# Kernel optimization log

Hardware: AMD Instinct MI355X
Metric: run time of the kernel (lower is better)

## Reference

```python
import jax, jax.numpy as jnp
import numpy as np

N_NODES = 50000
N_EDGES = 600000
D_IN = 128
D_OUT = 128


def setup_inputs() -> dict:
    key = jax.random.key(0)
    k1, k2, k3, k4 = jax.random.split(key, 4)
    x = jax.random.normal(k1, (N_NODES, D_IN), dtype=jnp.float32)
    edge_index = jax.random.randint(k2, (2, N_EDGES), 0, N_NODES, dtype=jnp.int64)
    edge_weight = jax.random.uniform(k3, (N_EDGES,), dtype=jnp.float32)
    W = jax.random.normal(k4, (D_IN, D_OUT), dtype=jnp.float32) * (1.0 / np.sqrt(D_IN))
    b = jnp.zeros((D_OUT,), dtype=jnp.float32)
    return {"x": x, "edge_index": edge_index, "edge_weight": edge_weight, "W": W, "b": b}


def reference(x, edge_index, edge_weight, W, b):
    # GCNConv (PyG semantics): add self-loops, symmetric deg^{-1/2} normalization,
    # linear transform, scatter-add to targets, bias; then ReLU. Dropout is
    # identity in eval mode.
    n = x.shape[0]
    loop = jnp.arange(n, dtype=edge_index.dtype)
    src = jnp.concatenate([edge_index[0], loop])  # message sources
    dst = jnp.concatenate([edge_index[1], loop])  # aggregation targets
    ew = jnp.concatenate([edge_weight, jnp.ones((n,), dtype=x.dtype)])
    # weighted in-degree on targets
    deg = jax.ops.segment_sum(ew, dst, num_segments=n)
    dinv = jnp.where(deg > 0, jax.lax.rsqrt(deg), jnp.zeros_like(deg))
    norm = dinv[src] * ew * dinv[dst]  # [E+N]
    h = x @ W  # [N, D_OUT]
    msg = h[src] * norm[:, None]  # [E+N, D_OUT]
    out = jax.ops.segment_sum(msg, dst, num_segments=n) + b
    return jax.nn.relu(out)
```

## Files before the change

### kernel.cpp

```cpp
#include <hip/hip_runtime.h>

#define N_NODES 50000
#define N_EDGES 600000
#define D 128
#define SCAN_B 256
#define NB ((N_NODES + SCAN_B - 1) / SCAN_B)
#define REP 4
#define FXSHIFT 44
#define GEMM_BLOCKS ((N_NODES + 63) / 64)
#define FILL_BLOCKS ((N_EDGES + 255) / 256)
#define ZERO_BLOCKS 392

typedef __attribute__((ext_vector_type(8))) short short8;
typedef __attribute__((ext_vector_type(4))) float f32x4;
typedef unsigned long long u64;

__device__ __forceinline__ ushort f2bf(float f) {
    unsigned u = __float_as_uint(f);
    unsigned r = (u + 0x7FFFu + ((u >> 16) & 1u)) >> 16;
    return (ushort)r;
}
__device__ __forceinline__ float bf2f(ushort h) {
    return __uint_as_float(((unsigned)h) << 16);
}

__device__ __forceinline__ void wfrag_body(int t, const float* __restrict__ W,
                                           ushort* __restrict__ wfh,
                                           ushort* __restrict__ wfl) {
    int lane = t & 63;
    int ks   = (t >> 6) & 3;
    int ct   = t >> 8;
    int n  = ct * 16 + (lane & 15);
    int k0 = ks * 32 + (lane >> 4) * 8;
    ushort hv[8], lv[8];
#pragma unroll
    for (int j = 0; j < 8; ++j) {
        float v = W[(k0 + j) * D + n];
        ushort hh = f2bf(v);
        hv[j] = hh;
        lv[j] = f2bf(v - bf2f(hh));
    }
    size_t base = (((size_t)ct * 4 + ks) * 64 + lane) * 8;
#pragma unroll
    for (int j = 0; j < 8; ++j) { wfh[base + j] = hv[j]; wfl[base + j] = lv[j]; }
}

__global__ void prep_kernel(ulonglong2* __restrict__ zp, int n2,
                            const float* __restrict__ W,
                            ushort* __restrict__ wfh, ushort* __restrict__ wfl) {
    if (blockIdx.x < ZERO_BLOCKS) {
        int i = blockIdx.x * 256 + threadIdx.x;
        if (i < n2) zp[i] = make_ulonglong2(0ull, 0ull);
    } else {
        wfrag_body((blockIdx.x - ZERO_BLOCKS) * 256 + threadIdx.x, W, wfh, wfl);
    }
}

__global__ void deg_cnt_kernel(const int* __restrict__ dst,
                               const float* __restrict__ ew,
                               u64* __restrict__ degp) {
    int e = blockIdx.x * 256 + threadIdx.x;
    if (e < N_EDGES) {
        int d = dst[e];
        int r = blockIdx.x & (REP - 1);
        u64 fx = (u64)llrintf(ew[e] * 16777216.0f);
        atomicAdd(&degp[(size_t)d * REP + r], (1ull << FXSHIFT) | fx);
    }
}

__global__ void scan_fused_kernel(const u64* __restrict__ degp,
                                  float* __restrict__ dinv,
                                  int* __restrict__ off,
                                  int* __restrict__ cursor,
                                  u64* __restrict__ flags) {
    __shared__ int s[SCAN_B];
    __shared__ int sbase_sh;
    int t = threadIdx.x;
    int i = blockIdx.x * SCAN_B + t;
    int v = 0;
    u64 pr[REP];
    if (i < N_NODES) {
        u64 fxsum = 0;
        int c = 0;
        const u64* dp = degp + (size_t)i * REP;
#pragma unroll
        for (int r = 0; r < REP; ++r) {
            pr[r] = dp[r];
            fxsum += pr[r] & ((1ull << FXSHIFT) - 1);
            c += (int)(pr[r] >> FXSHIFT);
        }
        float deg = 1.0f + (float)fxsum * (1.0f / 16777216.0f);
        dinv[i] = rsqrtf(deg);
        v = c;
    }
    s[t] = v;
    __syncthreads();
    for (int o = 1; o < SCAN_B; o <<= 1) {
        int x = (t >= o) ? s[t - o] : 0;
        __syncthreads();
        s[t] += x;
        __syncthreads();
    }
    int localExcl = s[t] - v;
    int blockSum  = s[SCAN_B - 1];

    if (t == 0) {
        __hip_atomic_store(&flags[blockIdx.x], (1ull << 62) | (u64)blockSum,
                           __ATOMIC_RELEASE, __HIP_MEMORY_SCOPE_AGENT);
    }
    if (t < 64) {
        u64 sum = 0;
        for (int j0 = 0; j0 < (int)blockIdx.x; j0 += 64) {
            int j = j0 + t;
            u64 f = 0;
            if (j < (int)blockIdx.x) {
                do {
                    f = __hip_atomic_load(&flags[j], __ATOMIC_ACQUIRE,
                                          __HIP_MEMORY_SCOPE_AGENT);
                } while (f == 0ull);
            }
            sum += f & ((1ull << 62) - 1);
        }
#pragma unroll
        for (int o = 32; o > 0; o >>= 1)
            sum += (u64)__shfl_xor((long long)sum, o);
        if (t == 0) sbase_sh = (int)sum;
    }
    __syncthreads();

    if (i < N_NODES) {
        int o = localExcl + sbase_sh;
        off[i] = o;
        int run = o;
        int* cp = cursor + (size_t)i * REP;
#pragma unroll
        for (int r = 0; r < REP; ++r) {
            cp[r] = run;
            run += (int)(pr[r] >> FXSHIFT);
        }
    }
    if (i == 0) off[N_NODES] = N_EDGES;
}

__global__ __launch_bounds__(256) void fused_fg_kernel(
        const float* __restrict__ x,
        const ushort* __restrict__ wfh, const ushort* __restrict__ wfl,
        ushort* __restrict__ hbf,
        const int* __restrict__ src, const int* __restrict__ dst,
        const float* __restrict__ ew, const float* __restrict__ dinv,
        int* __restrict__ cursor, u64* __restrict__ edge_s) {
    __shared__ __attribute__((aligned(16))) ushort xh[64 * 128];

    int t = threadIdx.x;
    int b = blockIdx.x;
    if (b < GEMM_BLOCKS) {
        int r0 = b * 64;
#pragma unroll
        for (int p = 0; p < 8; ++p) {
            int row  = p * 8 + (t >> 5);
            int g    = t & 31;
            int grow = r0 + row;
            float4 v = make_float4(0.f, 0.f, 0.f, 0.f);
            if (grow < N_NODES) v = ((const float4*)(x + (size_t)grow * D))[g];
            ushort4 hi;
            hi.x = f2bf(v.x); hi.y = f2bf(v.y); hi.z = f2bf(v.z); hi.w = f2bf(v.w);
            int bo = (row * 256 + g * 8) ^ ((row & 7) << 4);
            *(ushort4*)((char*)xh + bo) = hi;
        }
        __syncthreads();

        int w  = t >> 6;
        int l  = t & 63;
        int m  = l & 15;
        int gq = l >> 4;

        f32x4 acc[8];
#pragma unroll
        for (int ct = 0; ct < 8; ++ct) acc[ct] = (f32x4){0.f, 0.f, 0.f, 0.f};

#pragma unroll
        for (int ks = 0; ks < 4; ++ks) {
            int row = w * 16 + m;
            int bo  = (row * 256 + gq * 16 + ks * 64) ^ ((row & 7) << 4);
            short8 ah = *(const short8*)((const char*)xh + bo);
#pragma unroll
            for (int ct = 0; ct < 8; ++ct) {
                size_t fb = (((size_t)ct * 4 + ks) * 64 + l) * 8;
                short8 bh = *(const short8*)(wfh + fb);
                short8 bl = *(const short8*)(wfl + fb);
                acc[ct] = __builtin_amdgcn_mfma_f32_16x16x32_bf16(ah, bh, acc[ct], 0, 0, 0);
                acc[ct] = __builtin_amdgcn_mfma_f32_16x16x32_bf16(ah, bl, acc[ct], 0, 0, 0);
            }
        }

        int orow0 = r0 + w * 16 + gq * 4;
#pragma unroll
        for (int ct = 0; ct < 8; ++ct) {
#pragma unroll
            for (int r = 0; r < 4; ++r) {
                int row = orow0 + r;
                if (row < N_NODES) hbf[(size_t)row * D + ct * 16 + m] = f2bf(acc[ct][r]);
            }
        }
    } else {
        int fb = b - GEMM_BLOCKS;
        int e = fb * 256 + t;
        if (e >= N_EDGES) return;
        int s = src[e];
        int d = dst[e];
        int r = fb & (REP - 1);
        int pos = atomicAdd(&cursor[(size_t)d * REP + r], 1);
        float w = ew[e] * dinv[s] * dinv[d];
        edge_s[pos] = ((u64)__float_as_uint(w) << 32) | (unsigned)s;
    }
}

__global__ __launch_bounds__(256) void gather_kernel(
        const int* __restrict__ off, const u64* __restrict__ edge_s,
        const float* __restrict__ dinv,
        const ushort* __restrict__ hbf, const float* __restrict__ b,
        float* __restrict__ out) {
    int node = blockIdx.x * 4 + (threadIdx.x >> 6);
    if (node >= N_NODES) return;
    int lane = threadIdx.x & 63;
    int q  = lane >> 4;
    int fl = lane & 15;

    int begin = off[node];
    int end   = off[node + 1];
    float dd  = dinv[node];
    float sw  = dd * dd;

    float acc[8] = {0.f, 0.f, 0.f, 0.f, 0.f, 0.f, 0.f, 0.f};

    short8 sv = ((const short8*)(hbf + (size_t)node * D))[fl];
    if (q == 0) {
#pragma unroll
        for (int j = 0; j < 8; ++j) acc[j] = bf2f((ushort)sv[j]) * sw;
    }

    for (int j0 = begin; j0 < end; j0 += 64) {
        int nc = end - j0;
        if (nc > 64) nc = 64;
        u64 p = 0;
        if (lane < nc) p = edge_s[j0 + lane];
        int iters = (nc + 3) >> 2;
#pragma unroll 2
        for (int t = 0; t < iters; ++t) {
            int ei = t * 4 + q;
            u64 pe = __shfl((long long)p, ei);
            bool valid = ei < nc;
            int   ss = valid ? (int)(pe & 0xFFFFFFFFu) : 0;
            float ww = valid ? __uint_as_float((unsigned)(pe >> 32)) : 0.0f;
            short8 v = ((const short8*)(hbf + (size_t)ss * D))[fl];
#pragma unroll
            for (int j = 0; j < 8; ++j)
                acc[j] = fmaf(bf2f((ushort)v[j]), ww, acc[j]);
        }
    }

#pragma unroll
    for (int j = 0; j < 8; ++j) {
        acc[j] += __shfl_xor(acc[j], 16);
        acc[j] += __shfl_xor(acc[j], 32);
    }

    if (q == 0) {
        float4 b1 = ((const float4*)b)[fl * 2];
        float4 b2 = ((const float4*)b)[fl * 2 + 1];
        float4 o1 = make_float4(fmaxf(acc[0] + b1.x, 0.f), fmaxf(acc[1] + b1.y, 0.f),
                                fmaxf(acc[2] + b1.z, 0.f), fmaxf(acc[3] + b1.w, 0.f));
        float4 o2 = make_float4(fmaxf(acc[4] + b2.x, 0.f), fmaxf(acc[5] + b2.y, 0.f),
                                fmaxf(acc[6] + b2.z, 0.f), fmaxf(acc[7] + b2.w, 0.f));
        ((float4*)(out + (size_t)node * D))[fl * 2]     = o1;
        ((float4*)(out + (size_t)node * D))[fl * 2 + 1] = o2;
    }
}

__global__ void fb_init_kernel(float* __restrict__ deg) {
    int i = blockIdx.x * 256 + threadIdx.x;
    if (i < N_NODES) deg[i] = 1.0f;
}
__global__ void fb_deg_kernel(const int* __restrict__ dst, const float* __restrict__ ew,
                              float* __restrict__ deg) {
    int e = blockIdx.x * 256 + threadIdx.x;
    if (e < N_EDGES) atomicAdd(&deg[dst[e]], ew[e]);
}
__global__ void fb_dinv_kernel(const float* __restrict__ deg, float* __restrict__ dinv) {
    int i = blockIdx.x * 256 + threadIdx.x;
    if (i < N_NODES) {
        float d = deg[i];
        dinv[i] = (d > 0.0f) ? rsqrtf(d) : 0.0f;
    }
}
__global__ void fb_gemm_kernel(const float* __restrict__ x, const float* __restrict__ W,
                               float* __restrict__ h) {
    __shared__ float xs[2][D];
    int lr  = threadIdx.x >> 7;
    int col = threadIdx.x & 127;
    int row = blockIdx.x * 2 + lr;
    if (row < N_NODES) xs[lr][col] = x[(size_t)row * D + col];
    __syncthreads();
    if (row >= N_NODES) return;
    float acc = 0.0f;
#pragma unroll 8
    for (int k = 0; k < D; ++k) acc = fmaf(xs[lr][k], W[k * D + col], acc);
    h[(size_t)row * D + col] = acc;
}
__global__ void fb_scatter_kernel(const int* __restrict__ src, const int* __restrict__ dst,
                                  const float* __restrict__ ew, const float* __restrict__ dinv,
                                  const float* __restrict__ h, float* __restrict__ acc) {
    int e = blockIdx.x * 4 + (threadIdx.x >> 6);
    if (e >= N_EDGES) return;
    int lane = threadIdx.x & 63;
    int s = src[e];
    int d = dst[e];
    float w = ew[e] * dinv[s] * dinv[d];
    float2 v = ((const float2*)(h + (size_t)s * D))[lane];
    float* ap = acc + (size_t)d * D + lane * 2;
    atomicAdd(ap,     v.x * w);
    atomicAdd(ap + 1, v.y * w);
}
__global__ void fb_finalize_kernel(const float* __restrict__ h, const float* __restrict__ dinv,
                                   const float* __restrict__ b, float* __restrict__ out) {
    int i = blockIdx.x * 256 + threadIdx.x;
    if (i >= N_NODES * D) return;
    int node = i >> 7;
    int col  = i & 127;
    float di = dinv[node];
    float v = out[i] + h[i] * di * di + b[col];
    out[i] = fmaxf(v, 0.0f);
}

extern "C" void kernel_launch(void* const* d_in, const int* in_sizes, int n_in,
                              void* d_out, int out_size, void* d_ws, size_t ws_size,
                              hipStream_t stream) {
    const float* x  = (const float*)d_in[0];
    const int*   ei = (const int*)d_in[1];
    const float* ew = (const float*)d_in[2];
    const float* W  = (const float*)d_in[3];
    const float* b  = (const float*)d_in[4];
    float*       out = (float*)d_out;

    const int* src = ei;
    const int* dst = ei + N_EDGES;

    ushort* hbf    = (ushort*)d_ws;
    u64*    degp   = (u64*)(hbf + (size_t)N_NODES * D);
    u64*    flags  = degp + (size_t)REP * N_NODES;
    float*  dinv   = (float*)(flags + 256);
    int*    off    = (int*)(dinv + N_NODES);
    int*    cursor = off + (N_NODES + 2);
    u64*    edge_s = (u64*)(cursor + (size_t)REP * N_NODES);
    ushort* wfh    = (ushort*)(edge_s + N_EDGES);
    ushort* wfl    = wfh + 16384;
    size_t need = ((size_t)(wfl + 16384) - (size_t)d_ws);

    if (ws_size >= need) {
        int n2 = (int)(((size_t)REP * N_NODES * 8 + 256 * 8) / 16);
        prep_kernel<<<ZERO_BLOCKS + 8, 256, 0, stream>>>((ulonglong2*)degp, n2,
                                                         W, wfh, wfl);

        deg_cnt_kernel<<<FILL_BLOCKS, 256, 0, stream>>>(dst, ew, degp);

        scan_fused_kernel<<<NB, SCAN_B, 0, stream>>>(degp, dinv, off, cursor, flags);

        fused_fg_kernel<<<GEMM_BLOCKS + FILL_BLOCKS, 256, 0, stream>>>(
            x, wfh, wfl, hbf, src, dst, ew, dinv, cursor, edge_s);

        gather_kernel<<<(N_NODES + 3) / 4, 256, 0, stream>>>(off, edge_s, dinv,
                                                             hbf, b, out);
    } else {
        float* h    = (float*)d_ws;
        float* deg  = h + (size_t)N_NODES * D;
        float* dv   = deg + N_NODES;
        hipMemsetAsync(d_out, 0, (size_t)out_size * sizeof(float), stream);
        fb_init_kernel<<<(N_NODES + 255) / 256, 256, 0, stream>>>(deg);
        fb_deg_kernel<<<(N_EDGES + 255) / 256, 256, 0, stream>>>(dst, ew, deg);
        fb_dinv_kernel<<<(N_NODES + 255) / 256, 256, 0, stream>>>(deg, dv);
        fb_gemm_kernel<<<(N_NODES + 1) / 2, 256, 0, stream>>>(x, W, h);
        fb_scatter_kernel<<<(N_EDGES + 3) / 4, 256, 0, stream>>>(src, dst, ew, dv, h, out);
        fb_finalize_kernel<<<(N_NODES * D + 255) / 256, 256, 0, stream>>>(h, dv, b, out);
    }
}
```

Before: 112.3 us.

## Fuse all GCN stages into one cooperative persistent kernel with grid syncs

```diff
diff --git a/kernel.cpp b/kernel.cpp
--- a/kernel.cpp
+++ b/kernel.cpp
@@ -1,4 +1,6 @@
 #include <hip/hip_runtime.h>
+#include <hip/hip_cooperative_groups.h>
+namespace cg = cooperative_groups;
 
 #define N_NODES 50000
 #define N_EDGES 600000
@@ -9,6 +11,7 @@
 #define FXSHIFT 44
 #define GEMM_BLOCKS ((N_NODES + 63) / 64)
 #define FILL_BLOCKS ((N_EDGES + 255) / 256)
+#define GATHER_GROUPS ((N_NODES + 3) / 4)
 #define ZERO_BLOCKS 392
 
 typedef __attribute__((ext_vector_type(8))) short short8;
@@ -43,6 +46,228 @@
     size_t base = (((size_t)ct * 4 + ks) * 64 + lane) * 8;
 #pragma unroll
     for (int j = 0; j < 8; ++j) { wfh[base + j] = hv[j]; wfl[base + j] = lv[j]; }
+}
+
+__global__ __launch_bounds__(256) void mega_kernel(
+        const float* __restrict__ x, const int* __restrict__ src,
+        const int* __restrict__ dst, const float* __restrict__ ew,
+        const float* __restrict__ W, const float* __restrict__ bias,
+        ushort* __restrict__ hbf, u64* __restrict__ degp,
+        float* __restrict__ dinv, int* __restrict__ off,
+        int* __restrict__ cursor, u64* __restrict__ edge_s,
+        ushort* __restrict__ wfh, ushort* __restrict__ wfl,
+        int* __restrict__ blockSums, float* __restrict__ out) {
+    cg::grid_group grid = cg::this_grid();
+    const int nblk = gridDim.x;
+    const int b = blockIdx.x;
+    const int t = threadIdx.x;
+    __shared__ __attribute__((aligned(16))) ushort xh[64 * 128];
+    int* si = (int*)xh;
+
+    {
+        ulonglong2* zp = (ulonglong2*)degp;
+        const int n2 = REP * N_NODES / 2;
+        for (int i = b * 256 + t; i < n2; i += nblk * 256)
+            zp[i] = make_ulonglong2(0ull, 0ull);
+        if (b < 8) wfrag_body(b * 256 + t, W, wfh, wfl);
+    }
+    grid.sync();
+
+    for (int ch = b; ch < FILL_BLOCKS; ch += nblk) {
+        int e = ch * 256 + t;
+        if (e < N_EDGES) {
+            int d = dst[e];
+            int r = ch & (REP - 1);
+            u64 fx = (u64)llrintf(ew[e] * 16777216.0f);
+            atomicAdd(&degp[(size_t)d * REP + r], (1ull << FXSHIFT) | fx);
+        }
+    }
+    grid.sync();
+
+    int localExcl = 0, vcount = 0;
+    u64 pr[REP];
+    if (b < NB) {
+        int i = b * 256 + t;
+        if (i < N_NODES) {
+            u64 fxsum = 0;
+            int c = 0;
+            const u64* dp = degp + (size_t)i * REP;
+#pragma unroll
+            for (int r = 0; r < REP; ++r) {
+                pr[r] = dp[r];
+                fxsum += pr[r] & ((1ull << FXSHIFT) - 1);
+                c += (int)(pr[r] >> FXSHIFT);
+            }
+            dinv[i] = rsqrtf(1.0f + (float)fxsum * (1.0f / 16777216.0f));
+            vcount = c;
+        }
+        si[t] = vcount;
+        __syncthreads();
+        for (int o = 1; o < SCAN_B; o <<= 1) {
+            int xv = (t >= o) ? si[t - o] : 0;
+            __syncthreads();
+            si[t] += xv;
+            __syncthreads();
+        }
+        localExcl = si[t] - vcount;
+        if (t == SCAN_B - 1) blockSums[b] = si[t];
+    }
+    grid.sync();
+
+    if (b == 0) {
+        int val = (t < NB) ? blockSums[t] : 0;
+        si[t] = val;
+        __syncthreads();
+        for (int o = 1; o < SCAN_B; o <<= 1) {
+            int xv = (t >= o) ? si[t - o] : 0;
+            __syncthreads();
+            si[t] += xv;
+            __syncthreads();
+        }
+        if (t < NB) blockSums[t] = si[t] - val;
+    }
+    grid.sync();
+
+    if (b < NB) {
+        int i = b * 256 + t;
+        if (i < N_NODES) {
+            int o = localExcl + blockSums[b];
+            off[i] = o;
+            int run = o;
+            int* cp = cursor + (size_t)i * REP;
+#pragma unroll
+            for (int r = 0; r < REP; ++r) {
+                cp[r] = run;
+                run += (int)(pr[r] >> FXSHIFT);
+            }
+        }
+        if (b == 0 && t == 0) off[N_NODES] = N_EDGES;
+    }
+    grid.sync();
+
+    for (int it = b; it < GEMM_BLOCKS + FILL_BLOCKS; it += nblk) {
+        if (it < GEMM_BLOCKS) {
+            int r0 = it * 64;
+#pragma unroll
+            for (int p = 0; p < 8; ++p) {
+                int row  = p * 8 + (t >> 5);
+                int g    = t & 31;
+                int grow = r0 + row;
+                float4 v = make_float4(0.f, 0.f, 0.f, 0.f);
+                if (grow < N_NODES) v = ((const float4*)(x + (size_t)grow * D))[g];
+                ushort4 hi;
+                hi.x = f2bf(v.x); hi.y = f2bf(v.y); hi.z = f2bf(v.z); hi.w = f2bf(v.w);
+                int bo = (row * 256 + g * 8) ^ ((row & 7) << 4);
+                *(ushort4*)((char*)xh + bo) = hi;
+            }
+            __syncthreads();
+
+            int w  = t >> 6;
+            int l  = t & 63;
+            int m  = l & 15;
+            int gq = l >> 4;
+
+            f32x4 acc[8];
+#pragma unroll
+            for (int ct = 0; ct < 8; ++ct) acc[ct] = (f32x4){0.f, 0.f, 0.f, 0.f};
+
+#pragma unroll
+            for (int ks = 0; ks < 4; ++ks) {
+                int row = w * 16 + m;
+                int bo  = (row * 256 + gq * 16 + ks * 64) ^ ((row & 7) << 4);
+                short8 ah = *(const short8*)((const char*)xh + bo);
+#pragma unroll
+                for (int ct = 0; ct < 8; ++ct) {
+                    size_t fb = (((size_t)ct * 4 + ks) * 64 + l) * 8;
+                    short8 bh = *(const short8*)(wfh + fb);
+                    short8 bl = *(const short8*)(wfl + fb);
+                    acc[ct] = __builtin_amdgcn_mfma_f32_16x16x32_bf16(ah, bh, acc[ct], 0, 0, 0);
+                    acc[ct] = __builtin_amdgcn_mfma_f32_16x16x32_bf16(ah, bl, acc[ct], 0, 0, 0);
+                }
+            }
+
+            int orow0 = r0 + w * 16 + gq * 4;
+#pragma unroll
+            for (int ct = 0; ct < 8; ++ct) {
+#pragma unroll
+                for (int r = 0; r < 4; ++r) {
+                    int row = orow0 + r;
+                    if (row < N_NODES) hbf[(size_t)row * D + ct * 16 + m] = f2bf(acc[ct][r]);
+                }
+            }
+            __syncthreads();
+        } else {
+            int fc = it - GEMM_BLOCKS;
+            int e = fc * 256 + t;
+            if (e < N_EDGES) {
+                int s = src[e];
+                int d = dst[e];
+                int r = fc & (REP - 1);
+                int pos = atomicAdd(&cursor[(size_t)d * REP + r], 1);
+                float w = ew[e] * dinv[s] * dinv[d];
+                edge_s[pos] = ((u64)__float_as_uint(w) << 32) | (unsigned)s;
+            }
+        }
+    }
+    grid.sync();
+
+    for (int g = b; g < GATHER_GROUPS; g += nblk) {
+        int node = g * 4 + (t >> 6);
+        if (node >= N_NODES) continue;
+        int lane = t & 63;
+        int q  = lane >> 4;
+        int fl = lane & 15;
+
+        int begin = off[node];
+        int end   = off[node + 1];
+        float dd  = dinv[node];
+        float sw  = dd * dd;
+
+        float acc[8] = {0.f, 0.f, 0.f, 0.f, 0.f, 0.f, 0.f, 0.f};
+
+        short8 sv = ((const short8*)(hbf + (size_t)node * D))[fl];
+        if (q == 0) {
+#pragma unroll
+            for (int j = 0; j < 8; ++j) acc[j] = bf2f((ushort)sv[j]) * sw;
+        }
+
+        for (int j0 = begin; j0 < end; j0 += 64) {
+            int nc = end - j0;
+            if (nc > 64) nc = 64;
+            u64 p = 0;
+            if (lane < nc) p = edge_s[j0 + lane];
+            int iters = (nc + 3) >> 2;
+#pragma unroll 2
+            for (int k = 0; k < iters; ++k) {
+                int ei = k * 4 + q;
+                u64 pe = __shfl((long long)p, ei);
+                bool valid = ei < nc;
+                int   ss = valid ? (int)(pe & 0xFFFFFFFFu) : 0;
+                float ww = valid ? __uint_as_float((unsigned)(pe >> 32)) : 0.0f;
+                short8 v = ((const short8*)(hbf + (size_t)ss * D))[fl];
+#pragma unroll
+                for (int j = 0; j < 8; ++j)
+                    acc[j] = fmaf(bf2f((ushort)v[j]), ww, acc[j]);
+            }
+        }
+
+#pragma unroll
+        for (int j = 0; j < 8; ++j) {
+            acc[j] += __shfl_xor(acc[j], 16);
+            acc[j] += __shfl_xor(acc[j], 32);
+        }
+
+        if (q == 0) {
+            float4 b1 = ((const float4*)bias)[fl * 2];
+            float4 b2 = ((const float4*)bias)[fl * 2 + 1];
+            float4 o1 = make_float4(fmaxf(acc[0] + b1.x, 0.f), fmaxf(acc[1] + b1.y, 0.f),
+                                    fmaxf(acc[2] + b1.z, 0.f), fmaxf(acc[3] + b1.w, 0.f));
+            float4 o2 = make_float4(fmaxf(acc[4] + b2.x, 0.f), fmaxf(acc[5] + b2.y, 0.f),
+                                    fmaxf(acc[6] + b2.z, 0.f), fmaxf(acc[7] + b2.w, 0.f));
+            ((float4*)(out + (size_t)node * D))[fl * 2]     = o1;
+            ((float4*)(out + (size_t)node * D))[fl * 2 + 1] = o2;
+        }
+    }
 }
 
 __global__ void prep_kernel(ulonglong2* __restrict__ zp, int n2,
@@ -89,8 +314,7 @@
             fxsum += pr[r] & ((1ull << FXSHIFT) - 1);
             c += (int)(pr[r] >> FXSHIFT);
         }
-        float deg = 1.0f + (float)fxsum * (1.0f / 16777216.0f);
-        dinv[i] = rsqrtf(deg);
+        dinv[i] = rsqrtf(1.0f + (float)fxsum * (1.0f / 16777216.0f));
         v = c;
     }
     s[t] = v;
@@ -218,7 +442,7 @@
 __global__ __launch_bounds__(256) void gather_kernel(
         const int* __restrict__ off, const u64* __restrict__ edge_s,
         const float* __restrict__ dinv,
-        const ushort* __restrict__ hbf, const float* __restrict__ b,
+        const ushort* __restrict__ hbf, const float* __restrict__ bias,
         float* __restrict__ out) {
     int node = blockIdx.x * 4 + (threadIdx.x >> 6);
     if (node >= N_NODES) return;
@@ -246,8 +470,8 @@
         if (lane < nc) p = edge_s[j0 + lane];
         int iters = (nc + 3) >> 2;
 #pragma unroll 2
-        for (int t = 0; t < iters; ++t) {
-            int ei = t * 4 + q;
+        for (int k = 0; k < iters; ++k) {
+            int ei = k * 4 + q;
             u64 pe = __shfl((long long)p, ei);
             bool valid = ei < nc;
             int   ss = valid ? (int)(pe & 0xFFFFFFFFu) : 0;
@@ -266,8 +490,8 @@
     }
 
     if (q == 0) {
-        float4 b1 = ((const float4*)b)[fl * 2];
-        float4 b2 = ((const float4*)b)[fl * 2 + 1];
+        float4 b1 = ((const float4*)bias)[fl * 2];
+        float4 b2 = ((const float4*)bias)[fl * 2 + 1];
         float4 o1 = make_float4(fmaxf(acc[0] + b1.x, 0.f), fmaxf(acc[1] + b1.y, 0.f),
                                 fmaxf(acc[2] + b1.z, 0.f), fmaxf(acc[3] + b1.w, 0.f));
         float4 o2 = make_float4(fmaxf(acc[4] + b2.x, 0.f), fmaxf(acc[5] + b2.y, 0.f),
@@ -275,61 +499,6 @@
         ((float4*)(out + (size_t)node * D))[fl * 2]     = o1;
         ((float4*)(out + (size_t)node * D))[fl * 2 + 1] = o2;
     }
-}
-
-__global__ void fb_init_kernel(float* __restrict__ deg) {
-    int i = blockIdx.x * 256 + threadIdx.x;
-    if (i < N_NODES) deg[i] = 1.0f;
-}
-__global__ void fb_deg_kernel(const int* __restrict__ dst, const float* __restrict__ ew,
-                              float* __restrict__ deg) {
-    int e = blockIdx.x * 256 + threadIdx.x;
-    if (e < N_EDGES) atomicAdd(&deg[dst[e]], ew[e]);
-}
-__global__ void fb_dinv_kernel(const float* __restrict__ deg, float* __restrict__ dinv) {
-    int i = blockIdx.x * 256 + threadIdx.x;
-    if (i < N_NODES) {
-        float d = deg[i];
-        dinv[i] = (d > 0.0f) ? rsqrtf(d) : 0.0f;
-    }
-}
-__global__ void fb_gemm_kernel(const float* __restrict__ x, const float* __restrict__ W,
-                               float* __restrict__ h) {
-    __shared__ float xs[2][D];
-    int lr  = threadIdx.x >> 7;
-    int col = threadIdx.x & 127;
-    int row = blockIdx.x * 2 + lr;
-    if (row < N_NODES) xs[lr][col] = x[(size_t)row * D + col];
-    __syncthreads();
-    if (row >= N_NODES) return;
-    float acc = 0.0f;
-#pragma unroll 8
-    for (int k = 0; k < D; ++k) acc = fmaf(xs[lr][k], W[k * D + col], acc);
-    h[(size_t)row * D + col] = acc;
-}
-__global__ void fb_scatter_kernel(const int* __restrict__ src, const int* __restrict__ dst,
-                                  const float* __restrict__ ew, const float* __restrict__ dinv,
-                                  const float* __restrict__ h, float* __restrict__ acc) {
-    int e = blockIdx.x * 4 + (threadIdx.x >> 6);
-    if (e >= N_EDGES) return;
-    int lane = threadIdx.x & 63;
-    int s = src[e];
-    int d = dst[e];
-    float w = ew[e] * dinv[s] * dinv[d];
-    float2 v = ((const float2*)(h + (size_t)s * D))[lane];
-    float* ap = acc + (size_t)d * D + lane * 2;
-    atomicAdd(ap,     v.x * w);
-    atomicAdd(ap + 1, v.y * w);
-}
-__global__ void fb_finalize_kernel(const float* __restrict__ h, const float* __restrict__ dinv,
-                                   const float* __restrict__ b, float* __restrict__ out) {
-    int i = blockIdx.x * 256 + threadIdx.x;
-    if (i >= N_NODES * D) return;
-    int node = i >> 7;
-    int col  = i & 127;
-    float di = dinv[node];
-    float v = out[i] + h[i] * di * di + b[col];
-    out[i] = fmaxf(v, 0.0f);
 }
 
 extern "C" void kernel_launch(void* const* d_in, const int* in_sizes, int n_in,
@@ -339,7 +508,7 @@
     const int*   ei = (const int*)d_in[1];
     const float* ew = (const float*)d_in[2];
     const float* W  = (const float*)d_in[3];
-    const float* b  = (const float*)d_in[4];
+    const float* bias = (const float*)d_in[4];
     float*       out = (float*)d_out;
 
     const int* src = ei;
@@ -348,7 +517,8 @@
     ushort* hbf    = (ushort*)d_ws;
     u64*    degp   = (u64*)(hbf + (size_t)N_NODES * D);
     u64*    flags  = degp + (size_t)REP * N_NODES;
-    float*  dinv   = (float*)(flags + 256);
+    int*    blockSums = (int*)(flags + 256);
+    float*  dinv   = (float*)(blockSums + 256);
     int*    off    = (int*)(dinv + N_NODES);
     int*    cursor = off + (N_NODES + 2);
     u64*    edge_s = (u64*)(cursor + (size_t)REP * N_NODES);
@@ -356,30 +526,31 @@
     ushort* wfl    = wfh + 16384;
     size_t need = ((size_t)(wfl + 16384) - (size_t)d_ws);
 
-    if (ws_size >= need) {
+    if (ws_size < need) return;
+
+    int occ = 0;
+    hipError_t oe = hipOccupancyMaxActiveBlocksPerMultiprocessor(&occ, mega_kernel, 256, 0);
+    int grid = (oe == hipSuccess && occ > 0) ? occ * 256 : 1024;
+    if (grid > 2048) grid = 2048;
+    if (grid < SCAN_B) grid = SCAN_B;
+
+    void* args[] = {(void*)&x, (void*)&src, (void*)&dst, (void*)&ew, (void*)&W,
+                    (void*)&bias, (void*)&hbf, (void*)&degp, (void*)&dinv,
+                    (void*)&off, (void*)&cursor, (void*)&edge_s, (void*)&wfh,
+                    (void*)&wfl, (void*)&blockSums, (void*)&out};
+    hipError_t le = hipLaunchCooperativeKernel((const void*)mega_kernel,
+                                               dim3(grid), dim3(256), args, 0, stream);
+    if (le == hipSuccess) return;
+
+    {
         int n2 = (int)(((size_t)REP * N_NODES * 8 + 256 * 8) / 16);
         prep_kernel<<<ZERO_BLOCKS + 8, 256, 0, stream>>>((ulonglong2*)degp, n2,
                                                          W, wfh, wfl);
-
         deg_cnt_kernel<<<FILL_BLOCKS, 256, 0, stream>>>(dst, ew, degp);
-
         scan_fused_kernel<<<NB, SCAN_B, 0, stream>>>(degp, dinv, off, cursor, flags);
-
         fused_fg_kernel<<<GEMM_BLOCKS + FILL_BLOCKS, 256, 0, stream>>>(
             x, wfh, wfl, hbf, src, dst, ew, dinv, cursor, edge_s);
-
-        gather_kernel<<<(N_NODES + 3) / 4, 256, 0, stream>>>(off, edge_s, dinv,
-                                                             hbf, b, out);
-    } else {
-        float* h    = (float*)d_ws;
-        float* deg  = h + (size_t)N_NODES * D;
-        float* dv   = deg + N_NODES;
-        hipMemsetAsync(d_out, 0, (size_t)out_size * sizeof(float), stream);
-        fb_init_kernel<<<(N_NODES + 255) / 256, 256, 0, stream>>>(deg);
-        fb_deg_kernel<<<(N_EDGES + 255) / 256, 256, 0, stream>>>(dst, ew, deg);
-        fb_dinv_kernel<<<(N_NODES + 255) / 256, 256, 0, stream>>>(deg, dv);
-        fb_gemm_kernel<<<(N_NODES + 1) / 2, 256, 0, stream>>>(x, W, h);
-        fb_scatter_kernel<<<(N_EDGES + 3) / 4, 256, 0, stream>>>(src, dst, ew, dv, h, out);
-        fb_finalize_kernel<<<(N_NODES * D + 255) / 256, 256, 0, stream>>>(h, dv, b, out);
-    }
-}
+        gather_kernel<<<GATHER_GROUPS, 256, 0, stream>>>(off, edge_s, dinv,
+                                                         hbf, bias, out);
+    }
+}
```

Result: slower. 379.9 us (+238.3%).

## Split fused GEMM/fill kernel and stage W fragments in shared memory

Applied to the files above, without the earlier changes.

```diff
diff --git a/kernel.cpp b/kernel.cpp
--- a/kernel.cpp
+++ b/kernel.cpp
@@ -9,6 +9,7 @@
 #define FXSHIFT 44
 #define GEMM_BLOCKS ((N_NODES + 63) / 64)
 #define FILL_BLOCKS ((N_EDGES + 255) / 256)
+#define GATHER_GROUPS ((N_NODES + 3) / 4)
 #define ZERO_BLOCKS 392
 
 typedef __attribute__((ext_vector_type(8))) short short8;
@@ -89,8 +90,7 @@
             fxsum += pr[r] & ((1ull << FXSHIFT) - 1);
             c += (int)(pr[r] >> FXSHIFT);
         }
-        float deg = 1.0f + (float)fxsum * (1.0f / 16777216.0f);
-        dinv[i] = rsqrtf(deg);
+        dinv[i] = rsqrtf(1.0f + (float)fxsum * (1.0f / 16777216.0f));
         v = c;
     }
     s[t] = v;
@@ -142,83 +142,89 @@
     if (i == 0) off[N_NODES] = N_EDGES;
 }
 
-__global__ __launch_bounds__(256) void fused_fg_kernel(
+__global__ __launch_bounds__(256) void gemm_kernel(
         const float* __restrict__ x,
         const ushort* __restrict__ wfh, const ushort* __restrict__ wfl,
-        ushort* __restrict__ hbf,
-        const int* __restrict__ src, const int* __restrict__ dst,
-        const float* __restrict__ ew, const float* __restrict__ dinv,
-        int* __restrict__ cursor, u64* __restrict__ edge_s) {
+        ushort* __restrict__ hbf) {
     __shared__ __attribute__((aligned(16))) ushort xh[64 * 128];
-
-    int t = threadIdx.x;
-    int b = blockIdx.x;
-    if (b < GEMM_BLOCKS) {
-        int r0 = b * 64;
-#pragma unroll
-        for (int p = 0; p < 8; ++p) {
-            int row  = p * 8 + (t >> 5);
-            int g    = t & 31;
-            int grow = r0 + row;
-            float4 v = make_float4(0.f, 0.f, 0.f, 0.f);
-            if (grow < N_NODES) v = ((const float4*)(x + (size_t)grow * D))[g];
-            ushort4 hi;
-            hi.x = f2bf(v.x); hi.y = f2bf(v.y); hi.z = f2bf(v.z); hi.w = f2bf(v.w);
-            int bo = (row * 256 + g * 8) ^ ((row & 7) << 4);
-            *(ushort4*)((char*)xh + bo) = hi;
-        }
-        __syncthreads();
-
-        int w  = t >> 6;
-        int l  = t & 63;
-        int m  = l & 15;
-        int gq = l >> 4;
-
-        f32x4 acc[8];
-#pragma unroll
-        for (int ct = 0; ct < 8; ++ct) acc[ct] = (f32x4){0.f, 0.f, 0.f, 0.f};
-
-#pragma unroll
-        for (int ks = 0; ks < 4; ++ks) {
-            int row = w * 16 + m;
-            int bo  = (row * 256 + gq * 16 + ks * 64) ^ ((row & 7) << 4);
-            short8 ah = *(const short8*)((const char*)xh + bo);
-#pragma unroll
-            for (int ct = 0; ct < 8; ++ct) {
-                size_t fb = (((size_t)ct * 4 + ks) * 64 + l) * 8;
-                short8 bh = *(const short8*)(wfh + fb);
-                short8 bl = *(const short8*)(wfl + fb);
-                acc[ct] = __builtin_amdgcn_mfma_f32_16x16x32_bf16(ah, bh, acc[ct], 0, 0, 0);
-                acc[ct] = __builtin_amdgcn_mfma_f32_16x16x32_bf16(ah, bl, acc[ct], 0, 0, 0);
-            }
-        }
-
-        int orow0 = r0 + w * 16 + gq * 4;
+    __shared__ __attribute__((aligned(16))) ushort wsh[16384];
+    __shared__ __attribute__((aligned(16))) ushort wsl[16384];
+
+    int t  = threadIdx.x;
+    int r0 = blockIdx.x * 64;
+
+#pragma unroll
+    for (int p = 0; p < 8; ++p) {
+        int idx = p * 256 + t;
+        ((short8*)wsh)[idx] = ((const short8*)wfh)[idx];
+        ((short8*)wsl)[idx] = ((const short8*)wfl)[idx];
+    }
+#pragma unroll
+    for (int p = 0; p < 8; ++p) {
+        int row  = p * 8 + (t >> 5);
+        int g    = t & 31;
+        int grow = r0 + row;
+        float4 v = make_float4(0.f, 0.f, 0.f, 0.f);
+        if (grow < N_NODES) v = ((const float4*)(x + (size_t)grow * D))[g];
+        ushort4 hi;
+        hi.x = f2bf(v.x); hi.y = f2bf(v.y); hi.z = f2bf(v.z); hi.w = f2bf(v.w);
+        int bo = (row * 256 + g * 8) ^ ((row & 7) << 4);
+        *(ushort4*)((char*)xh + bo) = hi;
+    }
+    __syncthreads();
+
+    int w  = t >> 6;
+    int l  = t & 63;
+    int m  = l & 15;
+    int gq = l >> 4;
+
+    f32x4 acc[8];
+#pragma unroll
+    for (int ct = 0; ct < 8; ++ct) acc[ct] = (f32x4){0.f, 0.f, 0.f, 0.f};
+
+#pragma unroll
+    for (int ks = 0; ks < 4; ++ks) {
+        int row = w * 16 + m;
+        int bo  = (row * 256 + gq * 16 + ks * 64) ^ ((row & 7) << 4);
+        short8 ah = *(const short8*)((const char*)xh + bo);
 #pragma unroll
         for (int ct = 0; ct < 8; ++ct) {
-#pragma unroll
-            for (int r = 0; r < 4; ++r) {
-                int row = orow0 + r;
-                if (row < N_NODES) hbf[(size_t)row * D + ct * 16 + m] = f2bf(acc[ct][r]);
-            }
-        }
-    } else {
-        int fb = b - GEMM_BLOCKS;
-        int e = fb * 256 + t;
-        if (e >= N_EDGES) return;
-        int s = src[e];
-        int d = dst[e];
-        int r = fb & (REP - 1);
-        int pos = atomicAdd(&cursor[(size_t)d * REP + r], 1);
-        float w = ew[e] * dinv[s] * dinv[d];
-        edge_s[pos] = ((u64)__float_as_uint(w) << 32) | (unsigned)s;
-    }
+            int fb = ((ct * 4 + ks) * 64 + l);
+            short8 bh = ((const short8*)wsh)[fb];
+            short8 bl = ((const short8*)wsl)[fb];
+            acc[ct] = __builtin_amdgcn_mfma_f32_16x16x32_bf16(ah, bh, acc[ct], 0, 0, 0);
+            acc[ct] = __builtin_amdgcn_mfma_f32_16x16x32_bf16(ah, bl, acc[ct], 0, 0, 0);
+        }
+    }
+
+    int orow0 = r0 + w * 16 + gq * 4;
+#pragma unroll
+    for (int ct = 0; ct < 8; ++ct) {
+#pragma unroll
+        for (int r = 0; r < 4; ++r) {
+            int row = orow0 + r;
+            if (row < N_NODES) hbf[(size_t)row * D + ct * 16 + m] = f2bf(acc[ct][r]);
+        }
+    }
+}
+
+__global__ void fill_kernel(const int* __restrict__ src, const int* __restrict__ dst,
+                            const float* __restrict__ ew, const float* __restrict__ dinv,
+                            int* __restrict__ cursor, u64* __restrict__ edge_s) {
+    int e = blockIdx.x * 256 + threadIdx.x;
+    if (e >= N_EDGES) return;
+    int s = src[e];
+    int d = dst[e];
+    int r = blockIdx.x & (REP - 1);
+    int pos = atomicAdd(&cursor[(size_t)d * REP + r], 1);
+    float w = ew[e] * dinv[s] * dinv[d];
+    edge_s[pos] = ((u64)__float_as_uint(w) << 32) | (unsigned)s;
 }
 
 __global__ __launch_bounds__(256) void gather_kernel(
         const int* __restrict__ off, const u64* __restrict__ edge_s,
         const float* __restrict__ dinv,
-        const ushort* __restrict__ hbf, const float* __restrict__ b,
+        const ushort* __restrict__ hbf, const float* __restrict__ bias,
         float* __restrict__ out) {
     int node = blockIdx.x * 4 + (threadIdx.x >> 6);
     if (node >= N_NODES) return;
@@ -246,8 +252,8 @@
         if (lane < nc) p = edge_s[j0 + lane];
         int iters = (nc + 3) >> 2;
 #pragma unroll 2
-        for (int t = 0; t < iters; ++t) {
-            int ei = t * 4 + q;
+        for (int k = 0; k < iters; ++k) {
+            int ei = k * 4 + q;
             u64 pe = __shfl((long long)p, ei);
             bool valid = ei < nc;
             int   ss = valid ? (int)(pe & 0xFFFFFFFFu) : 0;
@@ -266,8 +272,8 @@
     }
 
     if (q == 0) {
-        float4 b1 = ((const float4*)b)[fl * 2];
-        float4 b2 = ((const float4*)b)[fl * 2 + 1];
+        float4 b1 = ((const float4*)bias)[fl * 2];
+        float4 b2 = ((const float4*)bias)[fl * 2 + 1];
         float4 o1 = make_float4(fmaxf(acc[0] + b1.x, 0.f), fmaxf(acc[1] + b1.y, 0.f),
                                 fmaxf(acc[2] + b1.z, 0.f), fmaxf(acc[3] + b1.w, 0.f));
         float4 o2 = make_float4(fmaxf(acc[4] + b2.x, 0.f), fmaxf(acc[5] + b2.y, 0.f),
@@ -275,61 +281,6 @@
         ((float4*)(out + (size_t)node * D))[fl * 2]     = o1;
         ((float4*)(out + (size_t)node * D))[fl * 2 + 1] = o2;
     }
-}
-
-__global__ void fb_init_kernel(float* __restrict__ deg) {
-    int i = blockIdx.x * 256 + threadIdx.x;
-    if (i < N_NODES) deg[i] = 1.0f;
-}
-__global__ void fb_deg_kernel(const int* __restrict__ dst, const float* __restrict__ ew,
-                              float* __restrict__ deg) {
-    int e = blockIdx.x * 256 + threadIdx.x;
-    if (e < N_EDGES) atomicAdd(&deg[dst[e]], ew[e]);
-}
-__global__ void fb_dinv_kernel(const float* __restrict__ deg, float* __restrict__ dinv) {
-    int i = blockIdx.x * 256 + threadIdx.x;
-    if (i < N_NODES) {
-        float d = deg[i];
-        dinv[i] = (d > 0.0f) ? rsqrtf(d) : 0.0f;
-    }
-}
-__global__ void fb_gemm_kernel(const float* __restrict__ x, const float* __restrict__ W,
-                               float* __restrict__ h) {
-    __shared__ float xs[2][D];
-    int lr  = threadIdx.x >> 7;
-    int col = threadIdx.x & 127;
-    int row = blockIdx.x * 2 + lr;
-    if (row < N_NODES) xs[lr][col] = x[(size_t)row * D + col];
-    __syncthreads();
-    if (row >= N_NODES) return;
-    float acc = 0.0f;
-#pragma unroll 8
-    for (int k = 0; k < D; ++k) acc = fmaf(xs[lr][k], W[k * D + col], acc);
-    h[(size_t)row * D + col] = acc;
-}
-__global__ void fb_scatter_kernel(const int* __restrict__ src, const int* __restrict__ dst,
-                                  const float* __restrict__ ew, const float* __restrict__ dinv,
-                                  const float* __restrict__ h, float* __restrict__ acc) {
-    int e = blockIdx.x * 4 + (threadIdx.x >> 6);
-    if (e >= N_EDGES) return;
-    int lane = threadIdx.x & 63;
-    int s = src[e];
-    int d = dst[e];
-    float w = ew[e] * dinv[s] * dinv[d];
-    float2 v = ((const float2*)(h + (size_t)s * D))[lane];
-    float* ap = acc + (size_t)d * D + lane * 2;
-    atomicAdd(ap,     v.x * w);
-    atomicAdd(ap + 1, v.y * w);
-}
-__global__ void fb_finalize_kernel(const float* __restrict__ h, const float* __restrict__ dinv,
-                                   const float* __restrict__ b, float* __restrict__ out) {
-    int i = blockIdx.x * 256 + threadIdx.x;
-    if (i >= N_NODES * D) return;
-    int node = i >> 7;
-    int col  = i & 127;
-    float di = dinv[node];
-    float v = out[i] + h[i] * di * di + b[col];
-    out[i] = fmaxf(v, 0.0f);
 }
 
 extern "C" void kernel_launch(void* const* d_in, const int* in_sizes, int n_in,
@@ -339,7 +290,7 @@
     const int*   ei = (const int*)d_in[1];
     const float* ew = (const float*)d_in[2];
     const float* W  = (const float*)d_in[3];
-    const float* b  = (const float*)d_in[4];
+    const float* bias = (const float*)d_in[4];
     float*       out = (float*)d_out;
 
     const int* src = ei;
@@ -355,31 +306,15 @@
     ushort* wfh    = (ushort*)(edge_s + N_EDGES);
     ushort* wfl    = wfh + 16384;
     size_t need = ((size_t)(wfl + 16384) - (size_t)d_ws);
-
-    if (ws_size >= need) {
-        int n2 = (int)(((size_t)REP * N_NODES * 8 + 256 * 8) / 16);
-        prep_kernel<<<ZERO_BLOCKS + 8, 256, 0, stream>>>((ulonglong2*)degp, n2,
-                                                         W, wfh, wfl);
-
-        deg_cnt_kernel<<<FILL_BLOCKS, 256, 0, stream>>>(dst, ew, degp);
-
-        scan_fused_kernel<<<NB, SCAN_B, 0, stream>>>(degp, dinv, off, cursor, flags);
-
-        fused_fg_kernel<<<GEMM_BLOCKS + FILL_BLOCKS, 256, 0, stream>>>(
-            x, wfh, wfl, hbf, src, dst, ew, dinv, cursor, edge_s);
-
-        gather_kernel<<<(N_NODES + 3) / 4, 256, 0, stream>>>(off, edge_s, dinv,
-                                                             hbf, b, out);
-    } else {
-        float* h    = (float*)d_ws;
-        float* deg  = h + (size_t)N_NODES * D;
-        float* dv   = deg + N_NODES;
-        hipMemsetAsync(d_out, 0, (size_t)out_size * sizeof(float), stream);
-        fb_init_kernel<<<(N_NODES + 255) / 256, 256, 0, stream>>>(deg);
-        fb_deg_kernel<<<(N_EDGES + 255) / 256, 256, 0, stream>>>(dst, ew, deg);
-        fb_dinv_kernel<<<(N_NODES + 255) / 256, 256, 0, stream>>>(deg, dv);
-        fb_gemm_kernel<<<(N_NODES + 1) / 2, 256, 0, stream>>>(x, W, h);
-        fb_scatter_kernel<<<(N_EDGES + 3) / 4, 256, 0, stream>>>(src, dst, ew, dv, h, out);
-        fb_finalize_kernel<<<(N_NODES * D + 255) / 256, 256, 0, stream>>>(h, dv, b, out);
-    }
-}
+    if (ws_size < need) return;
+
+    int n2 = (int)(((size_t)REP * N_NODES * 8 + 256 * 8) / 16);
+    prep_kernel<<<ZERO_BLOCKS + 8, 256, 0, stream>>>((ulonglong2*)degp, n2,
+                                                     W, wfh, wfl);
+    deg_cnt_kernel<<<FILL_BLOCKS, 256, 0, stream>>>(dst, ew, degp);
+    scan_fused_kernel<<<NB, SCAN_B, 0, stream>>>(degp, dinv, off, cursor, flags);
+    gemm_kernel<<<GEMM_BLOCKS, 256, 0, stream>>>(x, wfh, wfl, hbf);
+    fill_kernel<<<FILL_BLOCKS, 256, 0, stream>>>(src, dst, ew, dinv, cursor, edge_s);
+    gather_kernel<<<GATHER_GROUPS, 256, 0, stream>>>(off, edge_s, dinv,
+                                                     hbf, bias, out);
+}
```

Measured after the change: 123.8 us. 1.1x slower.
